# Performance work log

Measured on AMD Instinct MI355X. Metric: run time of the kernel, lower is better.

Reference implementation:

```python
import jax, jax.numpy as jnp
import numpy as np
from jax import lax

WINDOW_SIZE = 11
CHANNEL = 3
SIGMA = 1.5
C1 = 0.01 ** 2
C2 = 0.03 ** 2


def _create_window(window_size: int, channel: int) -> jnp.ndarray:
    g = jnp.arange(window_size, dtype=jnp.float32)
    g = jnp.exp(-(g - window_size // 2) ** 2 / (2.0 * SIGMA ** 2))
    g = g / g.sum()
    w2d = g[:, None] * g[None, :]                      # (K, K)
    # HWIO layout for grouped (depthwise) conv: (K, K, 1, channel)
    return jnp.tile(w2d[:, :, None, None], (1, 1, 1, channel))


def _dwconv(x: jnp.ndarray, window: jnp.ndarray) -> jnp.ndarray:
    pad = WINDOW_SIZE // 2
    return lax.conv_general_dilated(
        x, window,
        window_strides=(1, 1),
        padding=((pad, pad), (pad, pad)),
        dimension_numbers=("NCHW", "HWIO", "NCHW"),
        feature_group_count=CHANNEL,
    )


def setup_inputs() -> dict:
    key = jax.random.key(0)
    k1, k2 = jax.random.split(key)
    shape = (16, 3, 512, 512)
    img1 = jax.random.uniform(k1, shape, dtype=jnp.float32)
    img2 = jax.random.uniform(k2, shape, dtype=jnp.float32)
    window = _create_window(WINDOW_SIZE, CHANNEL)
    return {"img1": img1, "img2": img2, "window": window}


def reference(img1, img2, window):
    mu1 = _dwconv(img1, window)
    mu2 = _dwconv(img2, window)
    mu1_sq = mu1 * mu1
    mu2_sq = mu2 * mu2
    mu1_mu2 = mu1 * mu2
    sigma1_sq = _dwconv(img1 * img1, window) - mu1_sq
    sigma2_sq = _dwconv(img2 * img2, window) - mu2_sq
    sigma12 = _dwconv(img1 * img2, window) - mu1_mu2
    ssim_map = ((2.0 * mu1_mu2 + C1) * (2.0 * sigma12 + C2)) / (
        (mu1_sq + mu2_sq + C1) * (sigma1_sq + sigma2_sq + C2)
    )
    return ssim_map.mean()  # size_average=True
```

## Files before the change

kernel.cpp:

```cpp
#include <hip/hip_runtime.h>

#define KW 11
#define PAD 5
#define TW 32
#define TH 32
#define HROWS 16
#define ICOLS 42
#define S4 45
#define SX 45
#define IMH 512
#define IMW 512
#define NBLK 12288

typedef float f2 __attribute__((ext_vector_type(2)));
typedef float f4 __attribute__((ext_vector_type(4)));


#define PHASE_A(EDGE_, H_)                                                    \
    if (t < ICOLS * 4) {                                                      \
        const int c  = t % ICOLS;                                             \
        const int rg = t / ICOLS;                                   \
        const int r0 = rg * 4;                    \
        const int gr0 = iy0 + (H_) * HROWS + r0;                              \
        const int gc = ix0 + c;                                               \
        float a1[14], a2[14];                                                 \
        if (EDGE_) {                                                          \
            const bool cok = (gc >= 0) && (gc < IMW);                         \
            _Pragma("unroll")                                                 \
            for (int i = 0; i < 14; ++i) {                                    \
                const int gr = gr0 + i;                                       \
                const bool ok = cok && (gr >= 0) && (gr < IMH);               \
                const size_t o = base + (size_t)(ok ? gr : 0) * IMW           \
                               + (ok ? gc : 0);                               \
                a1[i] = ok ? img1[o] : 0.f;                                   \
                a2[i] = ok ? img2[o] : 0.f;                                   \
            }                                                                 \
        } else {                                                              \
                  \
            _Pragma("unroll")                                                 \
            for (int i = 0; i < 14; ++i) {                                    \
                const size_t o = base + (size_t)(gr0 + i) * IMW + gc;         \
                a1[i] = img1[o];                                              \
                a2[i] = img2[o];                                              \
            }                                                                 \
        }                                                                     \
        f2 m12[4]  = {{0,0},{0,0},{0,0},{0,0}};                               \
        f2 qq[4]   = {{0,0},{0,0},{0,0},{0,0}};                               \
        float sx[4] = {0, 0, 0, 0};                                           \
        _Pragma("unroll")                                                     \
        for (int i = 0; i < 14; ++i) {                                        \
            f2 x12; x12.x = a1[i]; x12.y = a2[i];                             \
            const f2 sq = x12 * x12;                                          \
            const float sxy = a1[i] * a2[i];                                  \
            _Pragma("unroll")                                                 \
            for (int k = 0; k < 4; ++k) {                                     \
                const int j = i - k;                                          \
                if (j >= 0 && j < KW) {                                       \
                    const float w = wg[j];                  \
                    const f2 w2 = {w, w};                                     \
                    m12[k] += w2 * x12;                     \
                    qq[k]  += w2 * sq;                      \
                    sx[k]  += w * sxy;                                        \
                }                                                             \
            }                                                                 \
        }                                                                     \
        _Pragma("unroll")                                                     \
        for (int k = 0; k < 4; ++k) {                                         \
            f4 v;                                                             \
            v.x = m12[k].x; v.y = m12[k].y;                                   \
            v.z = qq[k].x;  v.w = qq[k].y;                                    \
            vv4[(r0 + k) * S4 + c] = v;                    \
            vsx[(r0 + k) * SX + c] = sx[k];                \
        }                                                                     \
    }

#define PHASE_B(H_)                                                           \
    {                                                                         \
        const int row = t >> 4;                                    \
        const int cp  = t & 15;                           \
        const f4* __restrict__ p4 = &vv4[row * S4 + cp * 2];                  \
        const float* __restrict__ px = &vsx[row * SX + cp * 2];               \
        f2 am12[2] = {{0,0},{0,0}};                                           \
        f2 aqq[2]  = {{0,0},{0,0}};                                           \
        float asx[2] = {0, 0};                                                \
        _Pragma("unroll")                                                     \
        for (int b = 0; b < 2; ++b) {                                         \
            f4 v[6]; float vx[6];                                             \
            _Pragma("unroll")                                                 \
            for (int cc = 0; cc < 6; ++cc) {                                  \
                v[cc]  = p4[b * 6 + cc];                                      \
                vx[cc] = px[b * 6 + cc];                                      \
            }                                                                 \
            _Pragma("unroll")                                                 \
            for (int cc = 0; cc < 6; ++cc) {                                  \
                const int cg = b * 6 + cc;                                    \
                f2 v12; v12.x = v[cc].x; v12.y = v[cc].y;                     \
                f2 vqq; vqq.x = v[cc].z; vqq.y = v[cc].w;                     \
                _Pragma("unroll")                                             \
                for (int k = 0; k < 2; ++k) {                                 \
                    const int j = cg - k;                                     \
                    if (j >= 0 && j < KW) {                                   \
                        const float w = wg[j];                                \
                        const f2 w2 = {w, w};                                 \
                        am12[k] += w2 * v12;                                  \
                        aqq[k]  += w2 * vqq;                                  \
                        asx[k]  += w * vx[cc];                                \
                    }                                                         \
                }                                                             \
            }                                                                 \
        }                                                                     \
        _Pragma("unroll")                                                     \
        for (int k = 0; k < 2; ++k) {                                         \
            const float mu1 = am12[k].x, mu2 = am12[k].y;                     \
            const float mu1sq = mu1 * mu1, mu2sq = mu2 * mu2;                 \
            const float mu12 = mu1 * mu2;                                     \
            const float sig1 = aqq[k].x - mu1sq;                              \
            const float sig2 = aqq[k].y - mu2sq;                              \
            const float sig12 = asx[k] - mu12;                                \
            const float num = (2.f * mu12 + C1v) * (2.f * sig12 + C2v);       \
            const float den = (mu1sq + mu2sq + C1v) * (sig1 + sig2 + C2v);    \
            float r = __builtin_amdgcn_rcpf(den);                             \
            r = r * (2.f - den * r);               \
            lsum += num * r;                                                  \
        }                                                                     \
    }

__global__ __launch_bounds__(256, 4) void ssim_main(
    const float* __restrict__ img1, const float* __restrict__ img2,
    const float* __restrict__ window, float* __restrict__ partial)
{
    __shared__ f4 vv4[HROWS * S4];
    __shared__ float vsx[HROWS * SX];
    __shared__ float g[KW];
    __shared__ float wsum[4];

    const int t = threadIdx.x;

    if (t < KW) {
        float s = 0.f;
        for (int j = 0; j < KW; ++j) s += window[(t * KW + j) * 3];
        g[t] = s;
    }
    __syncthreads();

    float wg[KW];
#pragma unroll
    for (int j = 0; j < KW; ++j) {
        const int bi = __builtin_amdgcn_readfirstlane(__float_as_int(g[j]));
        wg[j] = __int_as_float(bi);
    }

    const float C1v = 0.0001f;
    const float C2v = 0.0009f;

    const int plane = blockIdx.z;
    const size_t base = (size_t)plane * IMH * IMW;
    const int ix0 = blockIdx.x * TW - PAD;
    const int iy0 = blockIdx.y * TH - PAD;

    const bool interior = (ix0 >= 0) && (ix0 + ICOLS <= IMW) &&
                          (iy0 >= 0) && (iy0 + TH + KW - 1 <= IMH);

    float lsum = 0.f;

    if (interior) { PHASE_A(false, 0) } else { PHASE_A(true, 0) }
    __syncthreads();
    PHASE_B(0)
    __syncthreads();
    if (interior) { PHASE_A(false, 1) } else { PHASE_A(true, 1) }
    __syncthreads();
    PHASE_B(1)

#pragma unroll
    for (int off = 32; off > 0; off >>= 1) lsum += __shfl_down(lsum, off, 64);
    if ((t & 63) == 0) wsum[t >> 6] = lsum;
    __syncthreads();
    if (t == 0) {
        unsigned bid = (blockIdx.z * gridDim.y + blockIdx.y) * gridDim.x
                     + blockIdx.x;
        partial[bid] = wsum[0] + wsum[1] + wsum[2] + wsum[3];
    }
}

__global__ __launch_bounds__(1024) void ssim_reduce(
    const float* __restrict__ partial, float* __restrict__ out, double inv_n)
{
    __shared__ double dsum[16];
    const int t = threadIdx.x;
    double s = 0.0;
    for (int i = t; i < NBLK; i += 1024) s += (double)partial[i];
#pragma unroll
    for (int off = 32; off > 0; off >>= 1) s += __shfl_down(s, off, 64);
    if ((t & 63) == 0) dsum[t >> 6] = s;
    __syncthreads();
    if (t == 0) {
        double tot = 0.0;
#pragma unroll
        for (int w = 0; w < 16; ++w) tot += dsum[w];
        out[0] = (float)(tot * inv_n);
    }
}

extern "C" void kernel_launch(void* const* d_in, const int* in_sizes, int n_in,
                              void* d_out, int out_size, void* d_ws, size_t ws_size,
                              hipStream_t stream) {
    const float* img1   = (const float*)d_in[0];
    const float* img2   = (const float*)d_in[1];
    const float* window = (const float*)d_in[2];
    float* out = (float*)d_out;
    float* partial = (float*)d_ws;

    const int nplanes = in_sizes[0] / (IMH * IMW);
    const long long total = (long long)in_sizes[0];

    dim3 grid(IMW / TW, IMH / TH, nplanes);
    ssim_main<<<grid, 256, 0, stream>>>(img1, img2, window, partial);
    ssim_reduce<<<1, 1024, 0, stream>>>(partial, out, 1.0 / (double)total);
}
```

Baseline: 170.9 us.

## Prefetch next half-tile global loads before horizontal pass and window setup

Splits the vertical-pass phase into a load step and a convolution step. The first half-tile's global loads are issued before the window-weight setup and barrier, and the second half's loads are issued before the horizontal pass of the first half, so memory latency overlaps with compute. The horizontal pass's LDS read batching also changes from 2x6 to 3x4. Holding 28 prefetched values live across the horizontal pass raises register pressure, which under launch_bounds(256,4) may cause spills or lower occupancy.

```diff
diff --git a/kernel.cpp b/kernel.cpp
--- a/kernel.cpp
+++ b/kernel.cpp
@@ -16,42 +16,41 @@
 typedef float f4 __attribute__((ext_vector_type(4)));
 
 
-#define PHASE_A(EDGE_, H_)                                                    \
-    if (t < ICOLS * 4) {                                                      \
-        const int c  = t % ICOLS;                                             \
-        const int rg = t / ICOLS;                                   \
-        const int r0 = rg * 4;                    \
-        const int gr0 = iy0 + (H_) * HROWS + r0;                              \
-        const int gc = ix0 + c;                                               \
-        float a1[14], a2[14];                                                 \
+#define A_LOAD(EDGE_, H_)                                                     \
+    if (aon) {                                                                \
+        const int gr0 = iy0 + (H_) * HROWS + ar0;                             \
         if (EDGE_) {                                                          \
-            const bool cok = (gc >= 0) && (gc < IMW);                         \
+            const bool cok = (agc >= 0) && (agc < IMW);                       \
             _Pragma("unroll")                                                 \
             for (int i = 0; i < 14; ++i) {                                    \
                 const int gr = gr0 + i;                                       \
                 const bool ok = cok && (gr >= 0) && (gr < IMH);               \
                 const size_t o = base + (size_t)(ok ? gr : 0) * IMW           \
-                               + (ok ? gc : 0);                               \
-                a1[i] = ok ? img1[o] : 0.f;                                   \
-                a2[i] = ok ? img2[o] : 0.f;                                   \
+                               + (ok ? agc : 0);                              \
+                p1[i] = ok ? img1[o] : 0.f;                                   \
+                p2[i] = ok ? img2[o] : 0.f;                                   \
             }                                                                 \
         } else {                                                              \
-                  \
+                   \
             _Pragma("unroll")                                                 \
             for (int i = 0; i < 14; ++i) {                                    \
-                const size_t o = base + (size_t)(gr0 + i) * IMW + gc;         \
-                a1[i] = img1[o];                                              \
-                a2[i] = img2[o];                                              \
-            }                                                                 \
-        }                                                                     \
+                const size_t o = base + (size_t)(gr0 + i) * IMW + agc;        \
+                p1[i] = img1[o];                                              \
+                p2[i] = img2[o];                                              \
+            }                                                                 \
+        }                                                                     \
+    }
+
+#define A_CONV(H_)                                                            \
+    if (aon) {                                                                \
         f2 m12[4]  = {{0,0},{0,0},{0,0},{0,0}};                               \
         f2 qq[4]   = {{0,0},{0,0},{0,0},{0,0}};                               \
         float sx[4] = {0, 0, 0, 0};                                           \
         _Pragma("unroll")                                                     \
         for (int i = 0; i < 14; ++i) {                                        \
-            f2 x12; x12.x = a1[i]; x12.y = a2[i];                             \
+            f2 x12; x12.x = p1[i]; x12.y = p2[i];                             \
             const f2 sq = x12 * x12;                                          \
-            const float sxy = a1[i] * a2[i];                                  \
+            const float sxy = p1[i] * p2[i];                                  \
             _Pragma("unroll")                                                 \
             for (int k = 0; k < 4; ++k) {                                     \
                 const int j = i - k;                                          \
@@ -69,8 +68,8 @@
             f4 v;                                                             \
             v.x = m12[k].x; v.y = m12[k].y;                                   \
             v.z = qq[k].x;  v.w = qq[k].y;                                    \
-            vv4[(r0 + k) * S4 + c] = v;                    \
-            vsx[(r0 + k) * SX + c] = sx[k];                \
+            vv4[(ar0 + k) * S4 + ac] = v;                  \
+            vsx[(ar0 + k) * SX + ac] = sx[k];              \
         }                                                                     \
     }
 
@@ -84,16 +83,16 @@
         f2 aqq[2]  = {{0,0},{0,0}};                                           \
         float asx[2] = {0, 0};                                                \
         _Pragma("unroll")                                                     \
-        for (int b = 0; b < 2; ++b) {                                         \
-            f4 v[6]; float vx[6];                                             \
-            _Pragma("unroll")                                                 \
-            for (int cc = 0; cc < 6; ++cc) {                                  \
-                v[cc]  = p4[b * 6 + cc];                                      \
-                vx[cc] = px[b * 6 + cc];                                      \
-            }                                                                 \
-            _Pragma("unroll")                                                 \
-            for (int cc = 0; cc < 6; ++cc) {                                  \
-                const int cg = b * 6 + cc;                                    \
+        for (int b = 0; b < 3; ++b) {                                         \
+            f4 v[4]; float vx[4];                                             \
+            _Pragma("unroll")                                                 \
+            for (int cc = 0; cc < 4; ++cc) {                                  \
+                v[cc]  = p4[b * 4 + cc];                                      \
+                vx[cc] = px[b * 4 + cc];                                      \
+            }                                                                 \
+            _Pragma("unroll")                                                 \
+            for (int cc = 0; cc < 4; ++cc) {                                  \
+                const int cg = b * 4 + cc;                                    \
                 f2 v12; v12.x = v[cc].x; v12.y = v[cc].y;                     \
                 f2 vqq; vqq.x = v[cc].z; vqq.y = v[cc].w;                     \
                 _Pragma("unroll")                                             \
@@ -136,6 +135,23 @@
 
     const int t = threadIdx.x;
 
+    const int plane = blockIdx.z;
+    const size_t base = (size_t)plane * IMH * IMW;
+    const int ix0 = blockIdx.x * TW - PAD;
+    const int iy0 = blockIdx.y * TH - PAD;
+
+    const bool aon = t < ICOLS * 4;
+    const int ac  = t % ICOLS;
+    const int ar0 = (t / ICOLS) * 4;
+    const int agc = ix0 + ac;
+
+    const bool interior = (ix0 >= 0) && (ix0 + ICOLS <= IMW) &&
+                          (iy0 >= 0) && (iy0 + TH + KW - 1 <= IMH);
+
+    float p1[14], p2[14];
+
+    if (interior) { A_LOAD(false, 0) } else { A_LOAD(true, 0) }
+
     if (t < KW) {
         float s = 0.f;
         for (int j = 0; j < KW; ++j) s += window[(t * KW + j) * 3];
@@ -152,22 +168,16 @@
 
     const float C1v = 0.0001f;
     const float C2v = 0.0009f;
-
-    const int plane = blockIdx.z;
-    const size_t base = (size_t)plane * IMH * IMW;
-    const int ix0 = blockIdx.x * TW - PAD;
-    const int iy0 = blockIdx.y * TH - PAD;
-
-    const bool interior = (ix0 >= 0) && (ix0 + ICOLS <= IMW) &&
-                          (iy0 >= 0) && (iy0 + TH + KW - 1 <= IMH);
-
     float lsum = 0.f;
 
-    if (interior) { PHASE_A(false, 0) } else { PHASE_A(true, 0) }
-    __syncthreads();
+    A_CONV(0)
+    __syncthreads();
+
+    if (interior) { A_LOAD(false, 1) } else { A_LOAD(true, 1) }
     PHASE_B(0)
     __syncthreads();
-    if (interior) { PHASE_A(false, 1) } else { PHASE_A(true, 1) }
+
+    A_CONV(1)
     __syncthreads();
     PHASE_B(1)
 
```

After: 170.3 us. No clear change (-0.3%).
